# Kernel tuning notes

Hardware: AMD Instinct MI355X
Metric: run time of the kernel (lower is better)

Reference implementation:

```python
import jax, jax.numpy as jnp
import numpy as np

N_NODES = 100000


def setup_inputs() -> dict:
    key = jax.random.key(0)
    k1, k2, k3 = jax.random.split(key, 3)
    pos = jax.random.normal(k1, (N_NODES, 2), dtype=jnp.float32)
    vel = jax.random.normal(k2, (N_NODES, 2), dtype=jnp.float32)
    edge_index = jax.random.randint(k3, (2, 6400000), 0, N_NODES, dtype=jnp.int64)
    return {"pos": pos, "vel": vel, "edge_index": edge_index}


def _forward(pos, vel, edge_index):
    n = pos.shape[0]
    h = jnp.concatenate([pos, vel], axis=1)  # [N,4]
    src, dst = edge_index[0], edge_index[1]  # PyG source_to_target: h_j=src, h_i=dst
    h_i = h[dst]  # [E,4] target
    h_j = h[src]  # [E,4] source
    x0, x1 = h_i[:, 0], h_i[:, 1]
    x4, x5 = h_j[:, 0], h_j[:, 1]
    d = x4 - x0
    m0 = (d + (x1 - x5) * 0.40914905) * 0.028998906
    m1 = (d + (x1 - x5) * 0.5819344) * -0.02637788
    m2 = (x1 * -0.07907551 - d) * -0.026721993
    m3 = (x1 * 0.95594215 - x5 - x0 * 0.20244296 - x4 * -0.17809269) * 0.026933579
    msg = jnp.stack([m0, m1, m2, m3], axis=1)  # [E,4]
    # zero messages where h_i == h_j exactly (e.g. self-loops)
    same = jnp.all(h_i - h_j == 0.0, axis=1)
    msg = jnp.where(same[:, None], 0.0, msg)
    mean_in, coll = msg[:, :2], msg[:, 2:]
    add_out = jax.ops.segment_sum(coll, dst, num_segments=n)          # add-reduce ch 2,3
    sum_mean = jax.ops.segment_sum(mean_in, dst, num_segments=n)
    cnt = jax.ops.segment_sum(jnp.ones_like(dst, dtype=msg.dtype), dst, num_segments=n)
    mean_out = jnp.where(cnt[:, None] > 0, sum_mean / jnp.maximum(cnt, 1.0)[:, None], 0.0)
    aggr = jnp.concatenate([add_out, mean_out], axis=1)  # [N,4]
    # update: x0..x3 = h, x4..x7 = aggr
    y0, y1, y2, y3 = h[:, 0], h[:, 1], h[:, 2], h[:, 3]
    y4, y5, y6, y7 = aggr[:, 0], aggr[:, 1], aggr[:, 2], aggr[:, 3]
    u0 = (y1 + y7 / 0.037233025) * -0.0020586958
    u1 = ((y0 - y7 ** 2 * y5) * 0.015168043 - y6) * -0.10450508
    u2 = (y7 - y1 * 0.027931638 + y6) * 0.075265266
    u3 = (y3 ** 2 - y6 + y2 - y3 + y7 * -0.33928046) * -0.08554904
    pred0 = (u0 + u3 + u0) * -0.24326763 - u1 / 0.7301285 - u2 * 1.1234615
    pred1 = u2 - (u1 + u0) + u3
    return jnp.stack([pred0, pred1], axis=1)  # [N,2]


def reference(pos, vel, edge_index):
    return _forward(pos, vel, edge_index)
```

## Files before the change

kernel.cpp:

```cpp
#include <hip/hip_runtime.h>

typedef int int4v __attribute__((ext_vector_type(4)));
typedef unsigned long long u64;
typedef unsigned int u32;

#define FSCALE 2048.0f
#define FBIAS  8.0f
#define BBITS  11
#define BSIZE  2048
#define MAXBKT 64
#define P1B    256
#define CAP    630
#define NSUB   32
#define SEGS   (P1B / NSUB)

__device__ __forceinline__ u64 pack_val(float2 ps, u32 same) {
    int fx = (int)rintf((ps.x + FBIAS) * FSCALE);
    int fy = (int)rintf((ps.y + FBIAS) * FSCALE);
    return (u64)(u32)fx | ((u64)(u32)fy << 22) | (1ULL << 44) | ((u64)same << 54);
}

__global__ __launch_bounds__(1024) void scatter_edges(
    const int4v* __restrict__ src4, const int4v* __restrict__ dst4, int nvec,
    const float2* __restrict__ pos,
    u32* __restrict__ records, u32* __restrict__ fills ,
    u64* __restrict__ acc_extra, int nbkt)
{
    __shared__ u32 cur[MAXBKT];
    const int blk = blockIdx.x;
    for (int i = threadIdx.x; i < nbkt; i += 1024) cur[i] = 0;
    __syncthreads();

    int span = (nvec + gridDim.x - 1) / gridDim.x;
    int lo = blk * span;
    int hi = lo + span; if (hi > nvec) hi = nvec;

    for (int i = lo + threadIdx.x; i < hi; i += 1024) {
        int4v s4 = __builtin_nontemporal_load(src4 + i);
        int4v d4 = __builtin_nontemporal_load(dst4 + i);
#pragma unroll
        for (int k = 0; k < 4; ++k) {
            u32 s = (u32)s4[k], d = (u32)d4[k];
            u32 b = d >> BBITS;
            u32 slot = __hip_atomic_fetch_add(&cur[b], 1u,
                           __ATOMIC_RELAXED, __HIP_MEMORY_SCOPE_WORKGROUP);
            if (slot < CAP) {
                u32 rec = s | ((d & (BSIZE - 1)) << 17) | ((u32)(s == d) << 28);
                records[((size_t)b * P1B + blk) * CAP + slot] = rec;
            } else {
                atomicAdd(acc_extra + d, pack_val(pos[s], (u32)(s == d)));
            }
        }
    }
    __syncthreads();
    for (int i = threadIdx.x; i < nbkt; i += 1024) {
        u32 c = cur[i]; if (c > CAP) c = CAP;
        fills[(size_t)i * P1B + blk] = c;
    }
}

__global__ __launch_bounds__(256) void reduce_buckets(
    u32* __restrict__ records, const u32* __restrict__ fills,
    const float2* __restrict__ pos, int nbkt)
{
    __shared__ u64 accl[BSIZE];
    int sub = blockIdx.x % NSUB;
    int b   = blockIdx.x / NSUB;
    for (int i = threadIdx.x; i < BSIZE; i += 256) accl[i] = 0;
    __syncthreads();

    const u32* fb = fills + (size_t)b * P1B + sub * SEGS;
    u32* rbase = records + ((size_t)b * P1B + sub * SEGS) * CAP;
#pragma unroll 1
    for (int j = 0; j < SEGS; ++j) {
        u32 count = fb[j];
        const u32* rp = rbase + (size_t)j * CAP;
        for (u32 r = threadIdx.x; r < count; r += 256) {
            u32 rec = rp[r];
            u32 s = rec & 0x1FFFF;
            u32 loc = (rec >> 17) & (BSIZE - 1);
            u64 val = pack_val(pos[s], rec >> 28);
            __hip_atomic_fetch_add(&accl[loc], val,
                                   __ATOMIC_RELAXED, __HIP_MEMORY_SCOPE_WORKGROUP);
        }
    }
    __syncthreads();
    u64* pdst = (u64*)rbase;
    for (int i = threadIdx.x; i < BSIZE; i += 256)
        pdst[i] = accl[i];
}

__global__ __launch_bounds__(256) void flock_edge_fb(
    const int4v* __restrict__ src4, const int4v* __restrict__ dst4, int nvec,
    const float2* __restrict__ pos, u64* __restrict__ acc)
{
    int tid = blockIdx.x * blockDim.x + threadIdx.x;
    int stride = gridDim.x * blockDim.x;
    for (int i = tid; i < nvec; i += stride) {
        int4v s4 = __builtin_nontemporal_load(src4 + i);
        int4v d4 = __builtin_nontemporal_load(dst4 + i);
#pragma unroll
        for (int k = 0; k < 4; ++k) {
            int s = s4[k], d = d4[k];
            atomicAdd(acc + d, pack_val(pos[s], (u32)(s == d)));
        }
    }
}

__global__ __launch_bounds__(256) void flock_node(
    const float2* __restrict__ pos, const float2* __restrict__ vel,
    const u32* __restrict__ records, const u64* __restrict__ acc_extra,
    int nsub, float2* __restrict__ out, int n_nodes)
{
    int n = blockIdx.x * blockDim.x + threadIdx.x;
    if (n >= n_nodes) return;

    u64 t = acc_extra[n];
    int b = n >> BBITS, loc = n & (BSIZE - 1);
    for (int k = 0; k < nsub; ++k) {
        const u64* p = (const u64*)(records + ((size_t)b * P1B + k * SEGS) * CAP);
        t += p[loc];
    }

    int fxi   = (int)(t & 0x3FFFFF);
    int fyi   = (int)((t >> 22) & 0x3FFFFF);
    int cnt_i = (int)((t >> 44) & 0x3FF);
    int sc_i  = (int)(t >> 54);

    float cnt = (float)cnt_i;
    float Sx  = (float)fxi * (1.0f / FSCALE) - FBIAS * cnt;
    float Sy  = (float)fyi * (1.0f / FSCALE) - FBIAS * cnt;
    float sc  = (float)sc_i;

    float2 p = pos[n];
    float2 v = vel[n];
    float x = p.x, y = p.y;

    float dsum = Sx - cnt * x;
    float esum = cnt * y - Sy;

    float sum_m0 = 0.028998906f * (dsum + esum * 0.40914905f);
    float sum_m1 = -0.02637788f * (dsum + esum * 0.5819344f);

    float sum_m3 = 0.026933579f *
        (cnt * (y * 0.95594215f - x * 0.20244296f) - Sy + 0.17809269f * Sx);
    sum_m3 -= sc * 0.026933579f *
        (y * 0.95594215f - y - x * 0.20244296f + 0.17809269f * x);

    float inv = cnt > 0.0f ? 1.0f / cnt : 0.0f;
    float y6 = sum_m0 * inv;
    float y7 = sum_m1 * inv;
    float y5 = sum_m3;

    float y0 = x, y1 = y, y2 = v.x, y3 = v.y;

    float u0 = (y1 + y7 / 0.037233025f) * -0.0020586958f;
    float u1 = ((y0 - y7 * y7 * y5) * 0.015168043f - y6) * -0.10450508f;
    float u2 = (y7 - y1 * 0.027931638f + y6) * 0.075265266f;
    float u3 = (y3 * y3 - y6 + y2 - y3 + y7 * -0.33928046f) * -0.08554904f;

    float pred0 = (u0 + u3 + u0) * -0.24326763f - u1 / 0.7301285f - u2 * 1.1234615f;
    float pred1 = u2 - (u1 + u0) + u3;

    out[n] = make_float2(pred0, pred1);
}

extern "C" void kernel_launch(void* const* d_in, const int* in_sizes, int n_in,
                              void* d_out, int out_size, void* d_ws, size_t ws_size,
                              hipStream_t stream) {
    const int n_nodes = in_sizes[0] / 2;
    const int n_edges = in_sizes[2] / 2;
    const float2* pos = (const float2*)d_in[0];
    const float2* vel = (const float2*)d_in[1];
    const int* ei = (const int*)d_in[2];
    const int* src = ei;
    const int* dst = ei + n_edges;
    const int nvec = n_edges / 4;

    const int nbkt = (n_nodes + BSIZE - 1) >> BBITS;
    const int node_stride = nbkt * BSIZE;

    u32* fills = (u32*)d_ws;
    u64* acc_extra = (u64*)((char*)d_ws + 65536);
    u32* records = (u32*)(acc_extra + node_stride);
    size_t need = 65536 + (size_t)node_stride * 8
                + (size_t)nbkt * P1B * CAP * 4;

    if (nbkt <= MAXBKT && ws_size >= need) {
        hipMemsetAsync(acc_extra, 0, (size_t)node_stride * 8, stream);
        scatter_edges<<<P1B, 1024, 0, stream>>>(
            (const int4v*)src, (const int4v*)dst, nvec, pos,
            records, fills, acc_extra, nbkt);
        reduce_buckets<<<nbkt * NSUB, 256, 0, stream>>>(
            records, fills, pos, nbkt);
        flock_node<<<(n_nodes + 255) / 256, 256, 0, stream>>>(
            pos, vel, records, acc_extra, NSUB, (float2*)d_out, n_nodes);
    } else {
        u64* acc_fb = (u64*)d_ws;
        hipMemsetAsync(acc_fb, 0, (size_t)n_nodes * 8, stream);
        int blocks = (nvec + 255) / 256;
        if (blocks > 2048) blocks = 2048;
        flock_edge_fb<<<blocks, 256, 0, stream>>>(
            (const int4v*)src, (const int4v*)dst, nvec, pos, acc_fb);
        flock_node<<<(n_nodes + 255) / 256, 256, 0, stream>>>(
            pos, vel, (const u32*)d_ws, acc_fb, 0, (float2*)d_out, n_nodes);
    }
}
```

Measured before the change: 90.79 us.

## Stage bucketed edge records in LDS and pre-quantize positions into packed u32

The scatter kernel now bins each tile of edges into per-bucket shared-memory staging arrays and then writes them out per wavefront in contiguous 64-record chunks, so the global record writes are coalesced instead of scattered per edge. A new prep kernel quantizes positions once into a 15+15-bit packed u32, which halves the size of the random gathers in the reduce kernel and removes the per-edge float conversion. This adds a kernel launch and extra synchronisation plus a serial prefix scan per tile. Clamping to 15 bits also narrows the representable range of positions.

Result: slower. 145.8 us (+60.6%).

```diff
diff --git a/kernel.cpp b/kernel.cpp
--- a/kernel.cpp
+++ b/kernel.cpp
@@ -13,55 +13,114 @@
 #define CAP    630
 #define NSUB   32
 #define SEGS   (P1B / NSUB)
-
-__device__ __forceinline__ u64 pack_val(float2 ps, u32 same) {
-    int fx = (int)rintf((ps.x + FBIAS) * FSCALE);
-    int fy = (int)rintf((ps.y + FBIAS) * FSCALE);
-    return (u64)(u32)fx | ((u64)(u32)fy << 22) | (1ULL << 44) | ((u64)same << 54);
+#define TILEV  1024
+#define SCAP   160
+
+__device__ __forceinline__ u64 qval(u32 q, u32 same) {
+    return (u64)(q & 0x7FFF) | ((u64)(q >> 15) << 22) | (1ULL << 44)
+         | ((u64)same << 54);
+}
+
+__global__ __launch_bounds__(256) void prep_pos(
+    const float2* __restrict__ pos, u32* __restrict__ qpos, int n)
+{
+    int i = blockIdx.x * blockDim.x + threadIdx.x;
+    if (i >= n) return;
+    float2 p = pos[i];
+    int fx = (int)rintf((p.x + FBIAS) * FSCALE);
+    int fy = (int)rintf((p.y + FBIAS) * FSCALE);
+    fx = min(max(fx, 0), 32767); fy = min(max(fy, 0), 32767);
+    qpos[i] = (u32)fx | ((u32)fy << 15);
 }
 
 __global__ __launch_bounds__(1024) void scatter_edges(
     const int4v* __restrict__ src4, const int4v* __restrict__ dst4, int nvec,
-    const float2* __restrict__ pos,
+    const u32* __restrict__ qpos,
     u32* __restrict__ records, u32* __restrict__ fills ,
     u64* __restrict__ acc_extra, int nbkt)
 {
-    __shared__ u32 cur[MAXBKT];
-    const int blk = blockIdx.x;
-    for (int i = threadIdx.x; i < nbkt; i += 1024) cur[i] = 0;
+    __shared__ u32 stage[MAXBKT][SCAP];
+    __shared__ u32 scnt[MAXBKT];
+    __shared__ u32 gbase[MAXBKT];
+    __shared__ u32 chbase[MAXBKT + 1];
+    const int blk = blockIdx.x, tid = threadIdx.x;
+    const int wid = tid >> 6, lane = tid & 63;
+
+    for (int i = tid; i < MAXBKT; i += 1024) gbase[i] = 0;
+
+    int spanv = (nvec + gridDim.x - 1) / gridDim.x;
+    int lov = blk * spanv;
+    int hiv = min(lov + spanv, nvec);
+
+    for (int vbase = lov; vbase < hiv; vbase += TILEV) {
+        if (tid < MAXBKT) scnt[tid] = 0;
+        __syncthreads();
+
+        int iv = vbase + tid;
+        if (iv < hiv) {
+            int4v s4 = __builtin_nontemporal_load(src4 + iv);
+            int4v d4 = __builtin_nontemporal_load(dst4 + iv);
+#pragma unroll
+            for (int k = 0; k < 4; ++k) {
+                u32 s = (u32)s4[k], d = (u32)d4[k];
+                u32 b = d >> BBITS;
+                u32 rec = s | ((d & (BSIZE - 1)) << 17) | ((u32)(s == d) << 28);
+                u32 idx = __hip_atomic_fetch_add(&scnt[b], 1u,
+                              __ATOMIC_RELAXED, __HIP_MEMORY_SCOPE_WORKGROUP);
+                if (idx < SCAP) {
+                    stage[b][idx] = rec;
+                } else {
+                    atomicAdd(acc_extra + d, qval(qpos[s], (u32)(s == d)));
+                }
+            }
+        }
+        __syncthreads();
+
+        if (tid == 0) {
+            u32 a = 0;
+            for (int b = 0; b < nbkt; ++b) {
+                chbase[b] = a;
+                u32 n = scnt[b]; if (n > SCAP) n = SCAP;
+                a += (n + 63) >> 6;
+            }
+            chbase[nbkt] = a;
+        }
+        __syncthreads();
+
+        u32 totch = chbase[nbkt];
+        for (u32 c = wid; c < totch; c += 16) {
+            int b = 0;
+            while (chbase[b + 1] <= c) ++b;
+            u32 j = c - chbase[b];
+            u32 n = scnt[b]; if (n > SCAP) n = SCAP;
+            u32 idx = (j << 6) + lane;
+            if (idx < n) {
+                u32 rec = stage[b][idx];
+                u32 g = gbase[b] + idx;
+                if (g < CAP) {
+                    records[((size_t)b * P1B + blk) * CAP + g] = rec;
+                } else {
+                    u32 d = ((u32)b << BBITS) | ((rec >> 17) & (BSIZE - 1));
+                    atomicAdd(acc_extra + d, qval(qpos[rec & 0x1FFFF], rec >> 28));
+                }
+            }
+        }
+        __syncthreads();
+        if (tid < MAXBKT) {
+            u32 n = scnt[tid]; if (n > SCAP) n = SCAP;
+            gbase[tid] += n;
+        }
+    }
     __syncthreads();
-
-    int span = (nvec + gridDim.x - 1) / gridDim.x;
-    int lo = blk * span;
-    int hi = lo + span; if (hi > nvec) hi = nvec;
-
-    for (int i = lo + threadIdx.x; i < hi; i += 1024) {
-        int4v s4 = __builtin_nontemporal_load(src4 + i);
-        int4v d4 = __builtin_nontemporal_load(dst4 + i);
-#pragma unroll
-        for (int k = 0; k < 4; ++k) {
-            u32 s = (u32)s4[k], d = (u32)d4[k];
-            u32 b = d >> BBITS;
-            u32 slot = __hip_atomic_fetch_add(&cur[b], 1u,
-                           __ATOMIC_RELAXED, __HIP_MEMORY_SCOPE_WORKGROUP);
-            if (slot < CAP) {
-                u32 rec = s | ((d & (BSIZE - 1)) << 17) | ((u32)(s == d) << 28);
-                records[((size_t)b * P1B + blk) * CAP + slot] = rec;
-            } else {
-                atomicAdd(acc_extra + d, pack_val(pos[s], (u32)(s == d)));
-            }
-        }
-    }
-    __syncthreads();
-    for (int i = threadIdx.x; i < nbkt; i += 1024) {
-        u32 c = cur[i]; if (c > CAP) c = CAP;
-        fills[(size_t)i * P1B + blk] = c;
+    for (int b = tid; b < nbkt; b += 1024) {
+        u32 g = gbase[b]; if (g > CAP) g = CAP;
+        fills[(size_t)b * P1B + blk] = g;
     }
 }
 
 __global__ __launch_bounds__(256) void reduce_buckets(
     u32* __restrict__ records, const u32* __restrict__ fills,
-    const float2* __restrict__ pos, int nbkt)
+    const u32* __restrict__ qpos, int nbkt)
 {
     __shared__ u64 accl[BSIZE];
     int sub = blockIdx.x % NSUB;
@@ -77,9 +136,8 @@
         const u32* rp = rbase + (size_t)j * CAP;
         for (u32 r = threadIdx.x; r < count; r += 256) {
             u32 rec = rp[r];
-            u32 s = rec & 0x1FFFF;
             u32 loc = (rec >> 17) & (BSIZE - 1);
-            u64 val = pack_val(pos[s], rec >> 28);
+            u64 val = qval(qpos[rec & 0x1FFFF], rec >> 28);
             __hip_atomic_fetch_add(&accl[loc], val,
                                    __ATOMIC_RELAXED, __HIP_MEMORY_SCOPE_WORKGROUP);
         }
@@ -102,7 +160,12 @@
 #pragma unroll
         for (int k = 0; k < 4; ++k) {
             int s = s4[k], d = d4[k];
-            atomicAdd(acc + d, pack_val(pos[s], (u32)(s == d)));
+            float2 ps = pos[s];
+            int fx = (int)rintf((ps.x + FBIAS) * FSCALE);
+            int fy = (int)rintf((ps.y + FBIAS) * FSCALE);
+            u64 val = (u64)(u32)fx | ((u64)(u32)fy << 22) | (1ULL << 44);
+            if (s == d) val |= (1ULL << 54);
+            atomicAdd(acc + d, val);
         }
     }
 }
@@ -182,17 +245,20 @@
 
     u32* fills = (u32*)d_ws;
     u64* acc_extra = (u64*)((char*)d_ws + 65536);
-    u32* records = (u32*)(acc_extra + node_stride);
-    size_t need = 65536 + (size_t)node_stride * 8
-                + (size_t)nbkt * P1B * CAP * 4;
+    size_t off_qpos = 65536 + (size_t)node_stride * 8;
+    u32* qpos = (u32*)((char*)d_ws + off_qpos);
+    size_t off_rec = (off_qpos + (size_t)n_nodes * 4 + 255) & ~(size_t)255;
+    u32* records = (u32*)((char*)d_ws + off_rec);
+    size_t need = off_rec + (size_t)nbkt * P1B * CAP * 4;
 
     if (nbkt <= MAXBKT && ws_size >= need) {
         hipMemsetAsync(acc_extra, 0, (size_t)node_stride * 8, stream);
+        prep_pos<<<(n_nodes + 255) / 256, 256, 0, stream>>>(pos, qpos, n_nodes);
         scatter_edges<<<P1B, 1024, 0, stream>>>(
-            (const int4v*)src, (const int4v*)dst, nvec, pos,
+            (const int4v*)src, (const int4v*)dst, nvec, qpos,
             records, fills, acc_extra, nbkt);
         reduce_buckets<<<nbkt * NSUB, 256, 0, stream>>>(
-            records, fills, pos, nbkt);
+            records, fills, qpos, nbkt);
         flock_node<<<(n_nodes + 255) / 256, 256, 0, stream>>>(
             pos, vel, records, acc_extra, NSUB, (float2*)d_out, n_nodes);
     } else {
```

## Prequantize positions into packed 32-bit table and batch record loads in reduction

Applied to the files above, without the earlier changes.

Adds a prep kernel that quantizes each node position once into a packed 15+15-bit word and zeroes the extra accumulator, replacing the memset. The scatter and reduction kernels then gather 4-byte quantized values instead of 8-byte float2 and skip the repeated rounding. The reduction loop is restructured to process two segments at once with paired record loads, issuing more independent gathers per thread to hide latency. Positions are clamped to 15 bits, which could differ from the old 22-bit fields for out-of-range values. It also adds an extra kernel launch.

Result: no change. 89.52 us (-1.4%).

```diff
diff --git a/kernel.cpp b/kernel.cpp
--- a/kernel.cpp
+++ b/kernel.cpp
@@ -1,6 +1,7 @@
 #include <hip/hip_runtime.h>
 
 typedef int int4v __attribute__((ext_vector_type(4)));
+typedef int int2v __attribute__((ext_vector_type(2)));
 typedef unsigned long long u64;
 typedef unsigned int u32;
 
@@ -14,15 +15,28 @@
 #define NSUB   32
 #define SEGS   (P1B / NSUB)
 
-__device__ __forceinline__ u64 pack_val(float2 ps, u32 same) {
-    int fx = (int)rintf((ps.x + FBIAS) * FSCALE);
-    int fy = (int)rintf((ps.y + FBIAS) * FSCALE);
-    return (u64)(u32)fx | ((u64)(u32)fy << 22) | (1ULL << 44) | ((u64)same << 54);
+__device__ __forceinline__ u64 qval(u32 q, u32 same) {
+    return (u64)(q & 0x7FFF) | ((u64)(q >> 15) << 22) | (1ULL << 44)
+         | ((u64)same << 54);
+}
+
+__global__ __launch_bounds__(256) void prep_pos(
+    const float2* __restrict__ pos, u32* __restrict__ qpos,
+    u64* __restrict__ acc_extra, int n, int node_stride)
+{
+    int i = blockIdx.x * blockDim.x + threadIdx.x;
+    if (i < node_stride) acc_extra[i] = 0;
+    if (i >= n) return;
+    float2 p = pos[i];
+    int fx = (int)rintf((p.x + FBIAS) * FSCALE);
+    int fy = (int)rintf((p.y + FBIAS) * FSCALE);
+    fx = min(max(fx, 0), 32767); fy = min(max(fy, 0), 32767);
+    qpos[i] = (u32)fx | ((u32)fy << 15);
 }
 
 __global__ __launch_bounds__(1024) void scatter_edges(
     const int4v* __restrict__ src4, const int4v* __restrict__ dst4, int nvec,
-    const float2* __restrict__ pos,
+    const u32* __restrict__ qpos,
     u32* __restrict__ records, u32* __restrict__ fills ,
     u64* __restrict__ acc_extra, int nbkt)
 {
@@ -33,7 +47,7 @@
 
     int span = (nvec + gridDim.x - 1) / gridDim.x;
     int lo = blk * span;
-    int hi = lo + span; if (hi > nvec) hi = nvec;
+    int hi = min(lo + span, nvec);
 
     for (int i = lo + threadIdx.x; i < hi; i += 1024) {
         int4v s4 = __builtin_nontemporal_load(src4 + i);
@@ -48,7 +62,7 @@
                 u32 rec = s | ((d & (BSIZE - 1)) << 17) | ((u32)(s == d) << 28);
                 records[((size_t)b * P1B + blk) * CAP + slot] = rec;
             } else {
-                atomicAdd(acc_extra + d, pack_val(pos[s], (u32)(s == d)));
+                atomicAdd(acc_extra + d, qval(qpos[s], (u32)(s == d)));
             }
         }
     }
@@ -59,9 +73,15 @@
     }
 }
 
+__device__ __forceinline__ void lds_add(u64* accl, u32 rec, u32 q) {
+    u32 loc = (rec >> 17) & (BSIZE - 1);
+    __hip_atomic_fetch_add(&accl[loc], qval(q, rec >> 28),
+                           __ATOMIC_RELAXED, __HIP_MEMORY_SCOPE_WORKGROUP);
+}
+
 __global__ __launch_bounds__(256) void reduce_buckets(
     u32* __restrict__ records, const u32* __restrict__ fills,
-    const float2* __restrict__ pos, int nbkt)
+    const u32* __restrict__ qpos, int nbkt)
 {
     __shared__ u64 accl[BSIZE];
     int sub = blockIdx.x % NSUB;
@@ -71,17 +91,36 @@
 
     const u32* fb = fills + (size_t)b * P1B + sub * SEGS;
     u32* rbase = records + ((size_t)b * P1B + sub * SEGS) * CAP;
+
 #pragma unroll 1
-    for (int j = 0; j < SEGS; ++j) {
-        u32 count = fb[j];
-        const u32* rp = rbase + (size_t)j * CAP;
-        for (u32 r = threadIdx.x; r < count; r += 256) {
-            u32 rec = rp[r];
-            u32 s = rec & 0x1FFFF;
-            u32 loc = (rec >> 17) & (BSIZE - 1);
-            u64 val = pack_val(pos[s], rec >> 28);
-            __hip_atomic_fetch_add(&accl[loc], val,
-                                   __ATOMIC_RELAXED, __HIP_MEMORY_SCOPE_WORKGROUP);
+    for (int j = 0; j < SEGS; j += 2) {
+        u32 c0 = fb[j], c1 = fb[j + 1];
+        const u32* rp0 = rbase + (size_t)j * CAP;
+        const u32* rp1 = rp0 + CAP;
+        u32 np0 = c0 >> 1, np1 = c1 >> 1;
+        u32 npmax = np0 > np1 ? np0 : np1;
+        for (u32 p = threadIdx.x; p < npmax; p += 256) {
+            bool a0 = p < np0, a1 = p < np1;
+            int2v ra, rb2;
+            if (a0) ra  = *(const int2v*)(rp0 + 2 * p);
+            if (a1) rb2 = *(const int2v*)(rp1 + 2 * p);
+            u32 q0 = 0, q1 = 0, q2 = 0, q3 = 0;
+            if (a0) { q0 = qpos[(u32)ra[0] & 0x1FFFF];
+                      q1 = qpos[(u32)ra[1] & 0x1FFFF]; }
+            if (a1) { q2 = qpos[(u32)rb2[0] & 0x1FFFF];
+                      q3 = qpos[(u32)rb2[1] & 0x1FFFF]; }
+            if (a0) { lds_add(accl, (u32)ra[0], q0);
+                      lds_add(accl, (u32)ra[1], q1); }
+            if (a1) { lds_add(accl, (u32)rb2[0], q2);
+                      lds_add(accl, (u32)rb2[1], q3); }
+        }
+        if ((c0 & 1) && threadIdx.x == 0) {
+            u32 rec = rp0[c0 - 1];
+            lds_add(accl, rec, qpos[rec & 0x1FFFF]);
+        }
+        if ((c1 & 1) && threadIdx.x == 1) {
+            u32 rec = rp1[c1 - 1];
+            lds_add(accl, rec, qpos[rec & 0x1FFFF]);
         }
     }
     __syncthreads();
@@ -102,7 +141,12 @@
 #pragma unroll
         for (int k = 0; k < 4; ++k) {
             int s = s4[k], d = d4[k];
-            atomicAdd(acc + d, pack_val(pos[s], (u32)(s == d)));
+            float2 ps = pos[s];
+            int fx = (int)rintf((ps.x + FBIAS) * FSCALE);
+            int fy = (int)rintf((ps.y + FBIAS) * FSCALE);
+            u64 val = (u64)(u32)fx | ((u64)(u32)fy << 22) | (1ULL << 44);
+            if (s == d) val |= (1ULL << 54);
+            atomicAdd(acc + d, val);
         }
     }
 }
@@ -182,17 +226,20 @@
 
     u32* fills = (u32*)d_ws;
     u64* acc_extra = (u64*)((char*)d_ws + 65536);
-    u32* records = (u32*)(acc_extra + node_stride);
-    size_t need = 65536 + (size_t)node_stride * 8
-                + (size_t)nbkt * P1B * CAP * 4;
+    size_t off_qpos = 65536 + (size_t)node_stride * 8;
+    u32* qpos = (u32*)((char*)d_ws + off_qpos);
+    size_t off_rec = (off_qpos + (size_t)n_nodes * 4 + 255) & ~(size_t)255;
+    u32* records = (u32*)((char*)d_ws + off_rec);
+    size_t need = off_rec + (size_t)nbkt * P1B * CAP * 4;
 
     if (nbkt <= MAXBKT && ws_size >= need) {
-        hipMemsetAsync(acc_extra, 0, (size_t)node_stride * 8, stream);
+        prep_pos<<<(node_stride + 255) / 256, 256, 0, stream>>>(
+            pos, qpos, acc_extra, n_nodes, node_stride);
         scatter_edges<<<P1B, 1024, 0, stream>>>(
-            (const int4v*)src, (const int4v*)dst, nvec, pos,
+            (const int4v*)src, (const int4v*)dst, nvec, qpos,
             records, fills, acc_extra, nbkt);
         reduce_buckets<<<nbkt * NSUB, 256, 0, stream>>>(
-            records, fills, pos, nbkt);
+            records, fills, qpos, nbkt);
         flock_node<<<(n_nodes + 255) / 256, 256, 0, stream>>>(
             pos, vel, records, acc_extra, NSUB, (float2*)d_out, n_nodes);
     } else {
```
